# Optimization experiments

Hardware: AMD Instinct MI355X
Metric: run time of the kernel (lower is better)

Reference implementation:

```python
import jax, jax.numpy as jnp
import numpy as np

IN_F = 128
OUT_F = 128


def setup_inputs() -> dict:
    key = jax.random.key(0)
    k_x, k_wb, k_bb, k_ww, k_bw = jax.random.split(key, 5)
    s = 1.0 / np.sqrt(IN_F)
    return {
        "x": jax.random.normal(k_x, (4, 2048, IN_F), dtype=jnp.float32),
        "Wb": jax.random.normal(k_wb, (IN_F, OUT_F), dtype=jnp.float32) * s,
        "bb": jax.random.normal(k_bb, (OUT_F,), dtype=jnp.float32) * s,
        "Ww": jax.random.normal(k_ww, (IN_F, IN_F * OUT_F), dtype=jnp.float32) * s,
        "bw": jax.random.normal(k_bw, (IN_F * OUT_F,), dtype=jnp.float32) * s,
    }


def reference(x, Wb, bb, Ww, bw):
    shape = x.shape
    xf = x.reshape(-1, IN_F)                      # [N, in]
    b = xf @ Wb + bb                              # [N, out]
    W = (xf @ Ww + bw).reshape(-1, IN_F, OUT_F)   # [N, in, out] (large)
    y = jnp.einsum('ni,nio->no', xf, W) + b       # batched vec-mat (M=1 bmm)
    return y.reshape(shape[:-1] + (OUT_F,))
```

## Files before the change

### kernel.cpp

```cpp
#include <hip/hip_runtime.h>
#include <stdint.h>
#include <stddef.h>


#define NROWS   8192
#define NKT     516
#define TILE_E  4096
#define XS_STRIDE 136
#define LS_STRIDE 136
#define BM      128
#define NSLICE  8

typedef unsigned short u16;
typedef short short8 __attribute__((ext_vector_type(8)));
typedef unsigned short ushort8 __attribute__((ext_vector_type(8)));
typedef float floatx4 __attribute__((ext_vector_type(4)));

__device__ __align__(16) u16   g_B[(size_t)NKT * TILE_E];
__device__ __align__(16) float g_P[(size_t)NSLICE * NROWS * 128];

__device__ __forceinline__ u16 f2bf_rne(float f) {
    unsigned int u = __float_as_uint(f);
    u += 0x7fffu + ((u >> 16) & 1u);
    return (u16)(u >> 16);
}

__global__ __launch_bounds__(256) void prep_kernel(
    const float* __restrict__ Ww, const float* __restrict__ Wb,
    const float* __restrict__ bw)
{
    __shared__ __align__(16) u16 ls[32 * LS_STRIDE];
    const int kt = blockIdx.x;
    const int t  = threadIdx.x;

    float v[16];
    if (kt < 512) {
        const float* src = Ww + (size_t)(kt >> 2)*16384 + (size_t)(kt & 3)*32*128 + t*16;
#pragma unroll
        for (int c = 0; c < 4; ++c) {
            const floatx4 f4 = *(const floatx4*)(src + c*4);
#pragma unroll
            for (int e = 0; e < 4; ++e) v[c*4 + e] = f4[e];
        }
    } else {
        const size_t base = (size_t)(kt - 512)*32*128 + t*16;
        const float* s1 = Wb + base;
        const float* s2 = bw + base;
#pragma unroll
        for (int c = 0; c < 4; ++c) {
            const floatx4 a = *(const floatx4*)(s1 + c*4);
            const floatx4 b = *(const floatx4*)(s2 + c*4);
#pragma unroll
            for (int e = 0; e < 4; ++e) v[c*4 + e] = a[e] + b[e];
        }
    }
    {
        const int kk = t >> 3;
        const int o0 = (t & 7) * 16;
        ushort8 w0, w1;
#pragma unroll
        for (int e = 0; e < 8; ++e) { w0[e] = f2bf_rne(v[e]); w1[e] = f2bf_rne(v[8+e]); }
        *(ushort8*)&ls[kk*LS_STRIDE + o0]     = w0;
        *(ushort8*)&ls[kk*LS_STRIDE + o0 + 8] = w1;
    }
    __syncthreads();
    {
        const int o   = t >> 1;
        const int kk0 = (t & 1) * 16;
        ushort8 w0, w1;
#pragma unroll
        for (int e = 0; e < 8; ++e) {
            w0[e] = ls[(kk0 + e)*LS_STRIDE + o];
            w1[e] = ls[(kk0 + 8 + e)*LS_STRIDE + o];
        }
        u16* outp = g_B + (size_t)kt*TILE_E + t*16;
        ((ushort8*)outp)[0] = w0; ((ushort8*)outp)[1] = w1;
    }
}

__global__ __launch_bounds__(512, 2) void gemm_kernel(const float* __restrict__ x)
{
    __shared__ __align__(16) u16 xs[BM * XS_STRIDE];

    const int b     = blockIdx.x;
    const int slice = b >> 6;
    const int rb    = b & 63;
    const int row0  = rb * BM;
    const int tid   = threadIdx.x;
    const int lane  = tid & 63;
    const int wave  = tid >> 6;
    const int wm    = wave >> 2;
    const int wc    = wave & 3;
    const int l15   = lane & 15;
    const int q     = lane >> 4;

#pragma unroll
    for (int it = 0; it < 4; ++it) {
        const int c  = it*512 + tid;
        const int r  = c >> 4;
        const int c8 = (c & 15) * 8;
        const float* sp = x + ((size_t)(row0 + r) << 7) + c8;
        const floatx4 f0 = *(const floatx4*)(sp);
        const floatx4 f1 = *(const floatx4*)(sp + 4);
        ushort8 w;
#pragma unroll
        for (int e = 0; e < 4; ++e) { w[e] = f2bf_rne(f0[e]); w[4+e] = f2bf_rne(f1[e]); }
        *(ushort8*)&xs[r*XS_STRIDE + c8] = w;
    }
    __syncthreads();

    short8 af[4][4];
#pragma unroll
    for (int ks = 0; ks < 4; ++ks)
#pragma unroll
        for (int mt = 0; mt < 4; ++mt)
            af[ks][mt] = *(const short8*)&xs[(wm*64 + mt*16 + l15)*XS_STRIDE + ks*32 + q*8];

    const floatx4 fzero = {0.f, 0.f, 0.f, 0.f};
    floatx4 acc[4][2];
#pragma unroll
    for (int i = 0; i < 4; ++i) { acc[i][0] = fzero; acc[i][1] = fzero; }

    const int p0 = slice*16 + (slice ? 1 : 0);
    const int np = slice ? 16 : 17;

    const int colbase = wc*32;
    const size_t loff = (size_t)(colbase + l15)*32 + q*8;
    const int ktN = (p0 + np)*4;

    auto LOADB = [&](int ktl, short8* dst) {
        const u16* tb = g_B + (size_t)ktl*TILE_E + loff;
        dst[0] = *(const short8*)(tb);
        dst[1] = *(const short8*)(tb + 512);
    };

    short8 Abuf[4][2], Bbuf[4][2];

#define DO_PHASE(CUR, NXT, PIDX, KTNXT)                                               \
    {                                                                                  \
        _Pragma("unroll")                                                              \
        for (int s = 0; s < 4; ++s) {                                                  \
            const int kl = (KTNXT) + s;                                                \
            LOADB(kl < ktN ? kl : ktN - 1, NXT[s]);                                    \
        }                                                                              \
        floatx4 aj[4][2];                                                              \
        _Pragma("unroll")                                                              \
        for (int mt = 0; mt < 4; ++mt) {                           \
            aj[mt][0] = __builtin_amdgcn_mfma_f32_16x16x32_bf16(af[0][mt], CUR[0][0], fzero, 0,0,0); \
            aj[mt][1] = __builtin_amdgcn_mfma_f32_16x16x32_bf16(af[0][mt], CUR[0][1], fzero, 0,0,0); \
        }                                                                              \
        _Pragma("unroll")                                                              \
        for (int mt = 0; mt < 4; ++mt) {                                               \
            aj[mt][0] = __builtin_amdgcn_mfma_f32_16x16x32_bf16(af[1][mt], CUR[1][0], aj[mt][0], 0,0,0); \
            aj[mt][1] = __builtin_amdgcn_mfma_f32_16x16x32_bf16(af[1][mt], CUR[1][1], aj[mt][1], 0,0,0); \
        }                                                                              \
        _Pragma("unroll")                                                              \
        for (int mt = 0; mt < 4; ++mt) {                                               \
            aj[mt][0] = __builtin_amdgcn_mfma_f32_16x16x32_bf16(af[2][mt], CUR[2][0], aj[mt][0], 0,0,0); \
            aj[mt][1] = __builtin_amdgcn_mfma_f32_16x16x32_bf16(af[2][mt], CUR[2][1], aj[mt][1], 0,0,0); \
        }                                                                              \
        _Pragma("unroll")                                                              \
        for (int mt = 0; mt < 4; ++mt) {                                               \
            aj[mt][0] = __builtin_amdgcn_mfma_f32_16x16x32_bf16(af[3][mt], CUR[3][0], aj[mt][0], 0,0,0); \
            aj[mt][1] = __builtin_amdgcn_mfma_f32_16x16x32_bf16(af[3][mt], CUR[3][1], aj[mt][1], 0,0,0); \
        }                                                                              \
        _Pragma("unroll")                                                              \
        for (int mt = 0; mt < 4; ++mt) {                                               \
            floatx4 xjv;                                                               \
            _Pragma("unroll")                                                          \
            for (int r = 0; r < 4; ++r) {                                              \
                const int rl = wm*64 + mt*16 + q*4 + r;      \
                xjv[r] = ((PIDX) < 128)                                                \
                    ? __uint_as_float(((unsigned int)xs[rl*XS_STRIDE + (PIDX)]) << 16) \
                    : 1.0f;                                                            \
            }                                                                          \
            acc[mt][0] += xjv * aj[mt][0];                                             \
            acc[mt][1] += xjv * aj[mt][1];                                             \
        }                                                                              \
    }

    int kt = p0*4;
#pragma unroll
    for (int s = 0; s < 4; ++s) LOADB(kt + s, Abuf[s]);

    const int pairs = np >> 1;
    for (int j = 0; j < pairs; ++j) {
        const int p = p0 + 2*j;
        DO_PHASE(Abuf, Bbuf, p,     kt + 4);
        DO_PHASE(Bbuf, Abuf, p + 1, kt + 8);
        kt += 8;
    }
    if (np & 1) {
        const int p = p0 + np - 1;
        DO_PHASE(Abuf, Bbuf, p, kt + 4);
    }
#undef DO_PHASE

    float* op = g_P + (size_t)slice * ((size_t)NROWS * 128);
#pragma unroll
    for (int mt = 0; mt < 4; ++mt)
#pragma unroll
        for (int nt = 0; nt < 2; ++nt) {
            const int col = colbase + nt*16 + l15;
#pragma unroll
            for (int r = 0; r < 4; ++r) {
                const int row = row0 + wm*64 + mt*16 + q*4 + r;
                op[((size_t)row << 7) + col] = acc[mt][nt][r];
            }
        }
}

__global__ __launch_bounds__(256) void finish_kernel(
    const float* __restrict__ bb, float* __restrict__ out)
{
    const int flat = (blockIdx.x*256 + threadIdx.x) * 8;
    floatx4 s0 = {0.f, 0.f, 0.f, 0.f};
    floatx4 s1 = {0.f, 0.f, 0.f, 0.f};
#pragma unroll
    for (int s = 0; s < NSLICE; ++s) {
        const float* p = g_P + (size_t)s * ((size_t)NROWS * 128) + flat;
        const floatx4 a = *(const floatx4*)p;
        const floatx4 c = *(const floatx4*)(p + 4);
#pragma unroll
        for (int e = 0; e < 4; ++e) { s0[e] += a[e]; s1[e] += c[e]; }
    }
    const floatx4 b0 = *(const floatx4*)(bb + (flat & 127));
    const floatx4 b1 = *(const floatx4*)(bb + (flat & 127) + 4);
    floatx4 o0, o1;
#pragma unroll
    for (int e = 0; e < 4; ++e) { o0[e] = s0[e] + b0[e]; o1[e] = s1[e] + b1[e]; }
    *(floatx4*)(out + flat)     = o0;
    *(floatx4*)(out + flat + 4) = o1;
}

extern "C" void kernel_launch(void* const* d_in, const int* in_sizes, int n_in,
                              void* d_out, int out_size, void* d_ws, size_t ws_size,
                              hipStream_t stream) {
    (void)in_sizes; (void)n_in; (void)out_size; (void)d_ws; (void)ws_size;
    const float* x  = (const float*)d_in[0];
    const float* Wb = (const float*)d_in[1];
    const float* bb = (const float*)d_in[2];
    const float* Ww = (const float*)d_in[3];
    const float* bw = (const float*)d_in[4];
    float* out = (float*)d_out;

    prep_kernel  <<<dim3(NKT),            dim3(256), 0, stream>>>(Ww, Wb, bw);
    gemm_kernel  <<<dim3(512),            dim3(512), 0, stream>>>(x);
    finish_kernel<<<dim3(NROWS*128/2048), dim3(256), 0, stream>>>(bb, out);
}
```

Baseline: 116.6 us.

## Stage B tiles into LDS via direct global-to-LDS loads with XOR swizzle

Replaces per-wave register prefetch of the B tiles from global memory with cooperative global_load_lds transfers into a double-buffered shared-memory staging area, synchronised by vmcnt waits and barriers. Both the prep-kernel output layout and the x tile in LDS switch to an XOR swizzle in place of row padding, to avoid bank conflicts. Each B tile is now fetched once per block and shared by the waves instead of loaded redundantly by each wave group. In exchange it adds two barriers per half-step and uses more LDS, which may reduce occupancy and serialise waves.

```diff
diff --git a/kernel.cpp b/kernel.cpp
--- a/kernel.cpp
+++ b/kernel.cpp
@@ -6,7 +6,6 @@
 #define NROWS   8192
 #define NKT     516
 #define TILE_E  4096
-#define XS_STRIDE 136
 #define LS_STRIDE 136
 #define BM      128
 #define NSLICE  8
@@ -15,6 +14,9 @@
 typedef short short8 __attribute__((ext_vector_type(8)));
 typedef unsigned short ushort8 __attribute__((ext_vector_type(8)));
 typedef float floatx4 __attribute__((ext_vector_type(4)));
+
+typedef __attribute__((address_space(1))) const unsigned int as1_u32;
+typedef __attribute__((address_space(3))) unsigned int as3_u32;
 
 __device__ __align__(16) u16   g_B[(size_t)NKT * TILE_E];
 __device__ __align__(16) float g_P[(size_t)NSLICE * NROWS * 128];
@@ -73,14 +75,17 @@
             w0[e] = ls[(kk0 + e)*LS_STRIDE + o];
             w1[e] = ls[(kk0 + 8 + e)*LS_STRIDE + o];
         }
-        u16* outp = g_B + (size_t)kt*TILE_E + t*16;
-        ((ushort8*)outp)[0] = w0; ((ushort8*)outp)[1] = w1;
+        u16* base = g_B + (size_t)kt*TILE_E;
+        const int swz = (o & 7) << 3;
+        *(ushort8*)&base[(o*32 + kk0    ) ^ swz] = w0;
+        *(ushort8*)&base[(o*32 + kk0 + 8) ^ swz] = w1;
     }
 }
 
 __global__ __launch_bounds__(512, 2) void gemm_kernel(const float* __restrict__ x)
 {
-    __shared__ __align__(16) u16 xs[BM * XS_STRIDE];
+    __shared__ __align__(16) u16 xs[128 * 128];
+    __shared__ __align__(16) u16 bs[2 * 2 * 4096];
 
     const int b     = blockIdx.x;
     const int slice = b >> 6;
@@ -105,7 +110,7 @@
         ushort8 w;
 #pragma unroll
         for (int e = 0; e < 4; ++e) { w[e] = f2bf_rne(f0[e]); w[4+e] = f2bf_rne(f1[e]); }
-        *(ushort8*)&xs[r*XS_STRIDE + c8] = w;
+        *(ushort8*)&xs[(r*128 + c8) ^ ((r & 7) << 3)] = w;
     }
     __syncthreads();
 
@@ -113,88 +118,86 @@
 #pragma unroll
     for (int ks = 0; ks < 4; ++ks)
 #pragma unroll
-        for (int mt = 0; mt < 4; ++mt)
-            af[ks][mt] = *(const short8*)&xs[(wm*64 + mt*16 + l15)*XS_STRIDE + ks*32 + q*8];
+        for (int mt = 0; mt < 4; ++mt) {
+            const int row = wm*64 + mt*16 + l15;
+            af[ks][mt] = *(const short8*)&xs[(row*128 + ks*32 + q*8) ^ ((l15 & 7) << 3)];
+        }
 
     const floatx4 fzero = {0.f, 0.f, 0.f, 0.f};
     floatx4 acc[4][2];
 #pragma unroll
     for (int i = 0; i < 4; ++i) { acc[i][0] = fzero; acc[i][1] = fzero; }
+    floatx4 aj[4][2];
 
     const int p0 = slice*16 + (slice ? 1 : 0);
     const int np = slice ? 16 : 17;
 
     const int colbase = wc*32;
-    const size_t loff = (size_t)(colbase + l15)*32 + q*8;
-    const int ktN = (p0 + np)*4;
-
-    auto LOADB = [&](int ktl, short8* dst) {
-        const u16* tb = g_B + (size_t)ktl*TILE_E + loff;
-        dst[0] = *(const short8*)(tb);
-        dst[1] = *(const short8*)(tb + 512);
-    };
-
-    short8 Abuf[4][2], Bbuf[4][2];
-
-#define DO_PHASE(CUR, NXT, PIDX, KTNXT)                                               \
+    const int swz8 = (l15 & 7) << 3;
+    const int idx0 = ((colbase + l15     ) * 32 + q*8) ^ swz8;
+    const int idx1 = ((colbase + l15 + 16) * 32 + q*8) ^ swz8;
+
+#define STAGE(BUF, KT)                                                                 \
     {                                                                                  \
+        const u16* g0 = g_B + (size_t)(KT)*TILE_E + (size_t)(wave*64 + lane)*8;        \
         _Pragma("unroll")                                                              \
-        for (int s = 0; s < 4; ++s) {                                                  \
-            const int kl = (KTNXT) + s;                                                \
-            LOADB(kl < ktN ? kl : ktN - 1, NXT[s]);                                    \
-        }                                                                              \
-        floatx4 aj[4][2];                                                              \
+        for (int i = 0; i < 2; ++i)                                                    \
+            __builtin_amdgcn_global_load_lds((as1_u32*)(g0 + i*4096),                  \
+                (as3_u32*)&bs[(BUF)*8192 + i*4096 + wave*512], 16, 0, 0);              \
+    }
+
+#define STEP(BUF, ISODD, DOISSUE, WN, PIDX, KTI)                                       \
+    {                                                                                  \
+        asm volatile("s_waitcnt vmcnt(%0)" :: "n"(WN) : "memory");                     \
+        __builtin_amdgcn_s_barrier();               \
+        short8 f0n0 = *(const short8*)&bs[(BUF)*8192        + idx0];                   \
+        short8 f0n1 = *(const short8*)&bs[(BUF)*8192        + idx1];                   \
+        short8 f1n0 = *(const short8*)&bs[(BUF)*8192 + 4096 + idx0];                   \
+        short8 f1n1 = *(const short8*)&bs[(BUF)*8192 + 4096 + idx1];                   \
+        asm volatile("s_waitcnt lgkmcnt(0)" ::: "memory");                             \
+        __builtin_amdgcn_s_barrier();          \
+        if (DOISSUE) STAGE(BUF, KTI);                                                  \
         _Pragma("unroll")                                                              \
-        for (int mt = 0; mt < 4; ++mt) {                           \
-            aj[mt][0] = __builtin_amdgcn_mfma_f32_16x16x32_bf16(af[0][mt], CUR[0][0], fzero, 0,0,0); \
-            aj[mt][1] = __builtin_amdgcn_mfma_f32_16x16x32_bf16(af[0][mt], CUR[0][1], fzero, 0,0,0); \
+        for (int mt = 0; mt < 4; ++mt) {                                               \
+            aj[mt][0] = __builtin_amdgcn_mfma_f32_16x16x32_bf16(af[(ISODD)*2][mt], f0n0, (ISODD) ? aj[mt][0] : fzero, 0,0,0); \
+            aj[mt][1] = __builtin_amdgcn_mfma_f32_16x16x32_bf16(af[(ISODD)*2][mt], f0n1, (ISODD) ? aj[mt][1] : fzero, 0,0,0); \
         }                                                                              \
         _Pragma("unroll")                                                              \
         for (int mt = 0; mt < 4; ++mt) {                                               \
-            aj[mt][0] = __builtin_amdgcn_mfma_f32_16x16x32_bf16(af[1][mt], CUR[1][0], aj[mt][0], 0,0,0); \
-            aj[mt][1] = __builtin_amdgcn_mfma_f32_16x16x32_bf16(af[1][mt], CUR[1][1], aj[mt][1], 0,0,0); \
+            aj[mt][0] = __builtin_amdgcn_mfma_f32_16x16x32_bf16(af[(ISODD)*2+1][mt], f1n0, aj[mt][0], 0,0,0); \
+            aj[mt][1] = __builtin_amdgcn_mfma_f32_16x16x32_bf16(af[(ISODD)*2+1][mt], f1n1, aj[mt][1], 0,0,0); \
         }                                                                              \
-        _Pragma("unroll")                                                              \
-        for (int mt = 0; mt < 4; ++mt) {                                               \
-            aj[mt][0] = __builtin_amdgcn_mfma_f32_16x16x32_bf16(af[2][mt], CUR[2][0], aj[mt][0], 0,0,0); \
-            aj[mt][1] = __builtin_amdgcn_mfma_f32_16x16x32_bf16(af[2][mt], CUR[2][1], aj[mt][1], 0,0,0); \
+        if (ISODD) {                                                                   \
+            _Pragma("unroll")                                                          \
+            for (int mt = 0; mt < 4; ++mt) {                                           \
+                floatx4 xjv;                                                           \
+                _Pragma("unroll")                                                      \
+                for (int r = 0; r < 4; ++r) {                                          \
+                    const int rl = wm*64 + mt*16 + q*4 + r;                            \
+                    xjv[r] = ((PIDX) < 128)                                            \
+                        ? __uint_as_float(((unsigned int)xs[(rl*128 + (PIDX)) ^ (((q*4 + r) & 7) << 3)]) << 16) \
+                        : 1.0f;                                                        \
+                }                                                                      \
+                acc[mt][0] += xjv * aj[mt][0];                                         \
+                acc[mt][1] += xjv * aj[mt][1];                                         \
+            }                                                                          \
         }                                                                              \
-        _Pragma("unroll")                                                              \
-        for (int mt = 0; mt < 4; ++mt) {                                               \
-            aj[mt][0] = __builtin_amdgcn_mfma_f32_16x16x32_bf16(af[3][mt], CUR[3][0], aj[mt][0], 0,0,0); \
-            aj[mt][1] = __builtin_amdgcn_mfma_f32_16x16x32_bf16(af[3][mt], CUR[3][1], aj[mt][1], 0,0,0); \
-        }                                                                              \
-        _Pragma("unroll")                                                              \
-        for (int mt = 0; mt < 4; ++mt) {                                               \
-            floatx4 xjv;                                                               \
-            _Pragma("unroll")                                                          \
-            for (int r = 0; r < 4; ++r) {                                              \
-                const int rl = wm*64 + mt*16 + q*4 + r;      \
-                xjv[r] = ((PIDX) < 128)                                                \
-                    ? __uint_as_float(((unsigned int)xs[rl*XS_STRIDE + (PIDX)]) << 16) \
-                    : 1.0f;                                                            \
-            }                                                                          \
-            acc[mt][0] += xjv * aj[mt][0];                                             \
-            acc[mt][1] += xjv * aj[mt][1];                                             \
-        }                                                                              \
     }
 
     int kt = p0*4;
-#pragma unroll
-    for (int s = 0; s < 4; ++s) LOADB(kt + s, Abuf[s]);
-
-    const int pairs = np >> 1;
-    for (int j = 0; j < pairs; ++j) {
-        const int p = p0 + 2*j;
-        DO_PHASE(Abuf, Bbuf, p,     kt + 4);
-        DO_PHASE(Bbuf, Abuf, p + 1, kt + 8);
-        kt += 8;
-    }
-    if (np & 1) {
-        const int p = p0 + np - 1;
-        DO_PHASE(Abuf, Bbuf, p, kt + 4);
-    }
-#undef DO_PHASE
+    STAGE(0, kt);
+    STAGE(1, kt + 2);
+
+    const int nh = np * 2;
+    for (int hh = 0; hh < nh - 2; hh += 2) {
+        STEP(0, 0, 1, 2, 0,               kt + 4);
+        STEP(1, 1, 1, 2, p0 + (hh >> 1),  kt + 6);
+        kt += 4;
+    }
+    STEP(0, 0, 0, 2, 0, 0);
+    STEP(1, 1, 0, 0, p0 + np - 1, 0);
+#undef STEP
+#undef STAGE
 
     float* op = g_P + (size_t)slice * ((size_t)NROWS * 128);
 #pragma unroll
```

New measurement: 136.7 us. 1.17x slower.

## Shrink row tile, rebalance K slices, add transposed x tile in LDS

Applied to the files above, without the earlier changes.

The GEMM block shrinks to 64 rows and 4 waves, and the K dimension is split into 6 slices instead of 8, giving 768 blocks. Half of the A fragments are now reloaded from LDS inside each phase instead of being held in registers, which lowers register pressure. A transposed bf16 copy of x in LDS lets the per-row x_j scale be read as one vector load instead of scattered scalar reads. The smaller tile halves B-operand reuse per block and so raises global/L2 traffic for the weight tiles, while fewer slices cut partial-sum traffic into the finish kernel.

```diff
diff --git a/kernel.cpp b/kernel.cpp
--- a/kernel.cpp
+++ b/kernel.cpp
@@ -7,13 +7,15 @@
 #define NKT     516
 #define TILE_E  4096
 #define XS_STRIDE 136
+#define XT_STRIDE 72
 #define LS_STRIDE 136
-#define BM      128
-#define NSLICE  8
+#define BM      64
+#define NSLICE  6
 
 typedef unsigned short u16;
 typedef short short8 __attribute__((ext_vector_type(8)));
 typedef unsigned short ushort8 __attribute__((ext_vector_type(8)));
+typedef unsigned short ushortx4 __attribute__((ext_vector_type(4)));
 typedef float floatx4 __attribute__((ext_vector_type(4)));
 
 __device__ __align__(16) u16   g_B[(size_t)NKT * TILE_E];
@@ -78,25 +80,24 @@
     }
 }
 
-__global__ __launch_bounds__(512, 2) void gemm_kernel(const float* __restrict__ x)
+__global__ __launch_bounds__(256, 2) void gemm_kernel(const float* __restrict__ x)
 {
     __shared__ __align__(16) u16 xs[BM * XS_STRIDE];
+    __shared__ __align__(16) u16 xt[128 * XT_STRIDE];
 
     const int b     = blockIdx.x;
-    const int slice = b >> 6;
-    const int rb    = b & 63;
+    const int slice = b >> 7;
+    const int rb    = b & 127;
     const int row0  = rb * BM;
     const int tid   = threadIdx.x;
     const int lane  = tid & 63;
     const int wave  = tid >> 6;
-    const int wm    = wave >> 2;
-    const int wc    = wave & 3;
     const int l15   = lane & 15;
     const int q     = lane >> 4;
 
 #pragma unroll
     for (int it = 0; it < 4; ++it) {
-        const int c  = it*512 + tid;
+        const int c  = it*256 + tid;
         const int r  = c >> 4;
         const int c8 = (c & 15) * 8;
         const float* sp = x + ((size_t)(row0 + r) << 7) + c8;
@@ -106,25 +107,27 @@
 #pragma unroll
         for (int e = 0; e < 4; ++e) { w[e] = f2bf_rne(f0[e]); w[4+e] = f2bf_rne(f1[e]); }
         *(ushort8*)&xs[r*XS_STRIDE + c8] = w;
+#pragma unroll
+        for (int e = 0; e < 8; ++e) xt[(c8 + e)*XT_STRIDE + r] = w[e];
     }
     __syncthreads();
 
-    short8 af[4][4];
-#pragma unroll
-    for (int ks = 0; ks < 4; ++ks)
+    short8 af01[2][4];
+#pragma unroll
+    for (int ks = 0; ks < 2; ++ks)
 #pragma unroll
         for (int mt = 0; mt < 4; ++mt)
-            af[ks][mt] = *(const short8*)&xs[(wm*64 + mt*16 + l15)*XS_STRIDE + ks*32 + q*8];
+            af01[ks][mt] = *(const short8*)&xs[(mt*16 + l15)*XS_STRIDE + ks*32 + q*8];
 
     const floatx4 fzero = {0.f, 0.f, 0.f, 0.f};
     floatx4 acc[4][2];
 #pragma unroll
     for (int i = 0; i < 4; ++i) { acc[i][0] = fzero; acc[i][1] = fzero; }
 
-    const int p0 = slice*16 + (slice ? 1 : 0);
-    const int np = slice ? 16 : 17;
-
-    const int colbase = wc*32;
+    const int p0 = slice*21 + (slice < 3 ? slice : 3);
+    const int np = 21 + (slice < 3 ? 1 : 0);
+
+    const int colbase = wave*32;
     const size_t loff = (size_t)(colbase + l15)*32 + q*8;
     const int ktN = (p0 + np)*4;
 
@@ -143,37 +146,46 @@
             const int kl = (KTNXT) + s;                                                \
             LOADB(kl < ktN ? kl : ktN - 1, NXT[s]);                                    \
         }                                                                              \
+        short8 af2[4], af3[4];                                                         \
+        _Pragma("unroll")                                                              \
+        for (int mt = 0; mt < 4; ++mt) {                                               \
+            af2[mt] = *(const short8*)&xs[(mt*16 + l15)*XS_STRIDE + 64 + q*8];         \
+            af3[mt] = *(const short8*)&xs[(mt*16 + l15)*XS_STRIDE + 96 + q*8];         \
+        }                                                                              \
+        const int pp_ = ((PIDX) < 128) ? (PIDX) : 0;                                   \
+        ushortx4 xjr[4];                                                               \
+        _Pragma("unroll")                                                              \
+        for (int mt = 0; mt < 4; ++mt)                                                 \
+            xjr[mt] = *(const ushortx4*)&xt[pp_*XT_STRIDE + mt*16 + q*4];              \
         floatx4 aj[4][2];                                                              \
         _Pragma("unroll")                                                              \
         for (int mt = 0; mt < 4; ++mt) {                           \
-            aj[mt][0] = __builtin_amdgcn_mfma_f32_16x16x32_bf16(af[0][mt], CUR[0][0], fzero, 0,0,0); \
-            aj[mt][1] = __builtin_amdgcn_mfma_f32_16x16x32_bf16(af[0][mt], CUR[0][1], fzero, 0,0,0); \
-        }                                                                              \
-        _Pragma("unroll")                                                              \
-        for (int mt = 0; mt < 4; ++mt) {                                               \
-            aj[mt][0] = __builtin_amdgcn_mfma_f32_16x16x32_bf16(af[1][mt], CUR[1][0], aj[mt][0], 0,0,0); \
-            aj[mt][1] = __builtin_amdgcn_mfma_f32_16x16x32_bf16(af[1][mt], CUR[1][1], aj[mt][1], 0,0,0); \
-        }                                                                              \
-        _Pragma("unroll")                                                              \
-        for (int mt = 0; mt < 4; ++mt) {                                               \
-            aj[mt][0] = __builtin_amdgcn_mfma_f32_16x16x32_bf16(af[2][mt], CUR[2][0], aj[mt][0], 0,0,0); \
-            aj[mt][1] = __builtin_amdgcn_mfma_f32_16x16x32_bf16(af[2][mt], CUR[2][1], aj[mt][1], 0,0,0); \
-        }                                                                              \
-        _Pragma("unroll")                                                              \
-        for (int mt = 0; mt < 4; ++mt) {                                               \
-            aj[mt][0] = __builtin_amdgcn_mfma_f32_16x16x32_bf16(af[3][mt], CUR[3][0], aj[mt][0], 0,0,0); \
-            aj[mt][1] = __builtin_amdgcn_mfma_f32_16x16x32_bf16(af[3][mt], CUR[3][1], aj[mt][1], 0,0,0); \
+            aj[mt][0] = __builtin_amdgcn_mfma_f32_16x16x32_bf16(af01[0][mt], CUR[0][0], fzero, 0,0,0); \
+            aj[mt][1] = __builtin_amdgcn_mfma_f32_16x16x32_bf16(af01[0][mt], CUR[0][1], fzero, 0,0,0); \
+        }                                                                              \
+        _Pragma("unroll")                                                              \
+        for (int mt = 0; mt < 4; ++mt) {                                               \
+            aj[mt][0] = __builtin_amdgcn_mfma_f32_16x16x32_bf16(af01[1][mt], CUR[1][0], aj[mt][0], 0,0,0); \
+            aj[mt][1] = __builtin_amdgcn_mfma_f32_16x16x32_bf16(af01[1][mt], CUR[1][1], aj[mt][1], 0,0,0); \
+        }                                                                              \
+        _Pragma("unroll")                                                              \
+        for (int mt = 0; mt < 4; ++mt) {                                               \
+            aj[mt][0] = __builtin_amdgcn_mfma_f32_16x16x32_bf16(af2[mt], CUR[2][0], aj[mt][0], 0,0,0); \
+            aj[mt][1] = __builtin_amdgcn_mfma_f32_16x16x32_bf16(af2[mt], CUR[2][1], aj[mt][1], 0,0,0); \
+        }                                                                              \
+        _Pragma("unroll")                                                              \
+        for (int mt = 0; mt < 4; ++mt) {                                               \
+            aj[mt][0] = __builtin_amdgcn_mfma_f32_16x16x32_bf16(af3[mt], CUR[3][0], aj[mt][0], 0,0,0); \
+            aj[mt][1] = __builtin_amdgcn_mfma_f32_16x16x32_bf16(af3[mt], CUR[3][1], aj[mt][1], 0,0,0); \
         }                                                                              \
         _Pragma("unroll")                                                              \
         for (int mt = 0; mt < 4; ++mt) {                                               \
             floatx4 xjv;                                                               \
             _Pragma("unroll")                                                          \
-            for (int r = 0; r < 4; ++r) {                                              \
-                const int rl = wm*64 + mt*16 + q*4 + r;      \
+            for (int r = 0; r < 4; ++r)                                                \
                 xjv[r] = ((PIDX) < 128)                                                \
-                    ? __uint_as_float(((unsigned int)xs[rl*XS_STRIDE + (PIDX)]) << 16) \
+                    ? __uint_as_float(((unsigned int)xjr[mt][r]) << 16)                \
                     : 1.0f;                                                            \
-            }                                                                          \
             acc[mt][0] += xjv * aj[mt][0];                                             \
             acc[mt][1] += xjv * aj[mt][1];                                             \
         }                                                                              \
@@ -204,7 +216,7 @@
             const int col = colbase + nt*16 + l15;
 #pragma unroll
             for (int r = 0; r < 4; ++r) {
-                const int row = row0 + wm*64 + mt*16 + q*4 + r;
+                const int row = row0 + mt*16 + q*4 + r;
                 op[((size_t)row << 7) + col] = acc[mt][nt][r];
             }
         }
@@ -245,6 +257,6 @@
     float* out = (float*)d_out;
 
     prep_kernel  <<<dim3(NKT),            dim3(256), 0, stream>>>(Ww, Wb, bw);
-    gemm_kernel  <<<dim3(512),            dim3(512), 0, stream>>>(x);
+    gemm_kernel  <<<dim3(768),            dim3(256), 0, stream>>>(x);
     finish_kernel<<<dim3(NROWS*128/2048), dim3(256), 0, stream>>>(bb, out);
 }
```

Result: slower. 124.4 us (+6.7%).
